# Performance work log

Measured on AMD Instinct MI355X. Metric: run time of the kernel, lower is better.

Reference implementation:

```python
import jax, jax.numpy as jnp
import numpy as np

E = 768
H = 12
D = E // H  # head_dim = 64
EPS = 1e-6
SCALE = D ** -0.5


def _l2norm(x, eps=EPS):
    # torch F.normalize: x / clamp_min(||x||_2, eps)
    n = jnp.sqrt(jnp.sum(x * x, axis=-1, keepdims=True))
    return x / jnp.maximum(n, eps)


def setup_inputs() -> dict:
    key = jax.random.key(0)
    ks = jax.random.split(key, 12)
    B, S = 2, 2048
    w = lambda k: jax.random.normal(k, (E, E), dtype=jnp.float32) * 0.02
    b = lambda k: jax.random.normal(k, (E,), dtype=jnp.float32) * 0.02
    return {
        "query": jax.random.normal(ks[0], (B, S, E), dtype=jnp.float32),
        "key": jax.random.normal(ks[1], (B, S, E), dtype=jnp.float32),
        "value": jax.random.normal(ks[2], (B, S, E), dtype=jnp.float32),
        "Wq": w(ks[3]), "bq": b(ks[4]),
        "Wk": w(ks[5]), "bk": b(ks[6]),
        "Wv": w(ks[7]), "bv": b(ks[8]),
        "Wo": w(ks[9]), "bo": b(ks[10]),
    }


def reference(query, key, value, Wq, bq, Wk, bk, Wv, bv, Wo, bo):
    B, T, _ = query.shape
    S = key.shape[1]
    # nn.Linear: x @ W.T + b; then split heads -> [B, H, S, D]
    split = lambda x, L: x.reshape(B, L, H, D).transpose(0, 2, 1, 3)
    q = split(query @ Wq.T + bq, T)
    k = split(key @ Wk.T + bk, S)
    v = split(value @ Wv.T + bv, S)
    q = _l2norm(q)
    k = _l2norm(k)
    scores = jnp.einsum("bhtd,bhsd->bhts", q, k) * SCALE
    attn = jax.nn.softmax(scores, axis=-1)
    ctx = jnp.einsum("bhts,bhsd->bhtd", attn, v)
    ctx = ctx.transpose(0, 2, 1, 3).reshape(B, T, E)
    return ctx @ Wo.T + bo
```

## Files before the change

### kernel.cpp

```cpp
#include <hip/hip_runtime.h>
#include <hip/hip_bf16.h>

#define EE 768
#define HH 12
#define DD 64
#define BB 2
#define SS 2048
#define MM (BB*SS)
#define NT (MM*EE)
#define NW (EE*EE)

typedef short short8 __attribute__((ext_vector_type(8)));
typedef float f32x4 __attribute__((ext_vector_type(4)));

static __device__ __forceinline__ unsigned short f2bf(float f) {
    unsigned int u = __float_as_uint(f);
    u += 0x7fffu + ((u >> 16) & 1u);
    return (unsigned short)(u >> 16);
}

static __device__ __forceinline__ void gl16(const void* g, void* l) {
    __builtin_amdgcn_global_load_lds(
        (const __attribute__((address_space(1))) unsigned int*)g,
        (__attribute__((address_space(3))) unsigned int*)l, 16, 0, 0);
}

static __device__ __forceinline__ int swz(int row, int chunk) {
    return row * 128 + ((chunk ^ (row & 7)) << 4);
}

__global__ __launch_bounds__(256) void cvt_x_kernel(
    const float* __restrict__ a0, const float* __restrict__ a1, const float* __restrict__ a2,
    unsigned short* __restrict__ o0, unsigned short* __restrict__ o1, unsigned short* __restrict__ o2)
{
    const float* s = (blockIdx.y == 0) ? a0 : (blockIdx.y == 1) ? a1 : a2;
    unsigned short* d = (blockIdx.y == 0) ? o0 : (blockIdx.y == 1) ? o1 : o2;
    const int idx = blockIdx.x * 256 + threadIdx.x;
    float4 f = ((const float4*)s)[idx];
    ushort4 u;
    u.x = f2bf(f.x); u.y = f2bf(f.y); u.z = f2bf(f.z); u.w = f2bf(f.w);
    ((ushort4*)d)[idx] = u;
}

__global__ __launch_bounds__(256) void cvt_w_kernel(
    const float* __restrict__ a0, const float* __restrict__ a1,
    const float* __restrict__ a2, const float* __restrict__ a3,
    unsigned short* __restrict__ o0, unsigned short* __restrict__ o1,
    unsigned short* __restrict__ o2, unsigned short* __restrict__ o3)
{
    const int y = blockIdx.y;
    const float* s = (y == 0) ? a0 : (y == 1) ? a1 : (y == 2) ? a2 : a3;
    unsigned short* d = (y == 0) ? o0 : (y == 1) ? o1 : (y == 2) ? o2 : o3;
    const int idx = blockIdx.x * 256 + threadIdx.x;
    float4 f = ((const float4*)s)[idx];
    ushort4 u;
    u.x = f2bf(f.x); u.y = f2bf(f.y); u.z = f2bf(f.z); u.w = f2bf(f.w);
    ((ushort4*)d)[idx] = u;
}

__global__ __launch_bounds__(256) void qkv_mfma_kernel(
    const unsigned short* __restrict__ xq, const unsigned short* __restrict__ xk,
    const unsigned short* __restrict__ xv,
    const unsigned short* __restrict__ Wq, const float* __restrict__ bq,
    const unsigned short* __restrict__ Wk, const float* __restrict__ bk,
    const unsigned short* __restrict__ Wv, const float* __restrict__ bv,
    unsigned short* __restrict__ qo, unsigned short* __restrict__ ko,
    unsigned short* __restrict__ vo)
{
    __shared__ short As[128 * 64];
    __shared__ short Bs[64 * 64];
    __shared__ float ssq[2][128];

    const int tid = threadIdx.x;
    const int bm  = blockIdx.x * 128;
    const int by  = blockIdx.y;
    const int proj = by / 12;
    const int h    = by % 12;
    const int n0r  = h * 64;

    const unsigned short* x = (proj == 0) ? xq : (proj == 1) ? xk : xv;
    const unsigned short* W = (proj == 0) ? Wq : (proj == 1) ? Wk : Wv;
    const float* bias       = (proj == 0) ? bq : (proj == 1) ? bk : bv;

    const int w  = tid >> 6;
    const int l  = tid & 63;
    const int c  = l & 15;
    const int g  = l >> 4;
    const int wm = w >> 1;
    const int wn = w & 1;
    const int lr8 = l >> 3;
    const int lc8 = (l & 7) ^ lr8;

    f32x4 acc[4][2] = {};

    for (int kt = 0; kt < EE; kt += 64) {
        __syncthreads();
        #pragma unroll
        for (int i = 0; i < 4; ++i) {
            const int t = w * 4 + i;
            const int row = t * 8 + lr8;
            gl16(x + (size_t)(bm + row) * EE + kt + lc8 * 8,
                 (unsigned short*)As + t * 512);
        }
        #pragma unroll
        for (int i = 0; i < 2; ++i) {
            const int t = w * 2 + i;
            const int row = t * 8 + lr8;
            gl16(W + (size_t)(n0r + row) * EE + kt + lc8 * 8,
                 (unsigned short*)Bs + t * 512);
        }
        __syncthreads();

        #pragma unroll
        for (int ks = 0; ks < 2; ++ks) {
            short8 bfr[2], afr[4];
            #pragma unroll
            for (int nt = 0; nt < 2; ++nt)
                bfr[nt] = *(const short8*)((const char*)Bs + swz(wn * 32 + nt * 16 + c, ks * 4 + g));
            #pragma unroll
            for (int mt = 0; mt < 4; ++mt)
                afr[mt] = *(const short8*)((const char*)As + swz(wm * 64 + mt * 16 + c, ks * 4 + g));
            #pragma unroll
            for (int mt = 0; mt < 4; ++mt)
                #pragma unroll
                for (int nt = 0; nt < 2; ++nt)
                    acc[mt][nt] = __builtin_amdgcn_mfma_f32_16x16x32_bf16(
                        afr[mt], bfr[nt], acc[mt][nt], 0, 0, 0);
        }
    }
    __syncthreads();

    float bb[2];
    #pragma unroll
    for (int nt = 0; nt < 2; ++nt) bb[nt] = bias[n0r + wn * 32 + nt * 16 + c];

    const int bidx  = bm >> 11;
    const int sbase = bm & (SS - 1);

    if (proj < 2) {
        f32x4 vr[4][2];
        f32x4 ssp[4];
        #pragma unroll
        for (int mt = 0; mt < 4; ++mt) {
            #pragma unroll
            for (int nt = 0; nt < 2; ++nt)
                #pragma unroll
                for (int j = 0; j < 4; ++j)
                    vr[mt][nt][j] = acc[mt][nt][j] + bb[nt];
            #pragma unroll
            for (int j = 0; j < 4; ++j)
                ssp[mt][j] = vr[mt][0][j]*vr[mt][0][j] + vr[mt][1][j]*vr[mt][1][j];
            #pragma unroll
            for (int j = 0; j < 4; ++j) {
                float s = ssp[mt][j];
                #pragma unroll
                for (int msk = 1; msk < 16; msk <<= 1) s += __shfl_xor(s, msk);
                ssp[mt][j] = s;
            }
        }
        if (c == 0) {
            #pragma unroll
            for (int mt = 0; mt < 4; ++mt)
                #pragma unroll
                for (int j = 0; j < 4; ++j)
                    ssq[wn][wm * 64 + mt * 16 + g * 4 + j] = ssp[mt][j];
        }
        __syncthreads();
        unsigned short* dst = (proj == 0) ? qo : ko;
        const float fold = (proj == 0) ? 0.125f : 1.0f;
        #pragma unroll
        for (int mt = 0; mt < 4; ++mt) {
            #pragma unroll
            for (int j = 0; j < 4; ++j) {
                const int rloc = wm * 64 + mt * 16 + g * 4 + j;
                const float ss = ssq[0][rloc] + ssq[1][rloc];
                const float inv = fold / fmaxf(sqrtf(ss), 1e-6f);
                const size_t base =
                    ((size_t)(bidx * HH + h) * SS + sbase + rloc) * DD;
                #pragma unroll
                for (int nt = 0; nt < 2; ++nt)
                    dst[base + wn * 32 + nt * 16 + c] = f2bf(vr[mt][nt][j] * inv);
            }
        }
    } else {
        #pragma unroll
        for (int mt = 0; mt < 4; ++mt)
            #pragma unroll
            for (int nt = 0; nt < 2; ++nt)
                #pragma unroll
                for (int j = 0; j < 4; ++j) {
                    const int row = wm * 64 + mt * 16 + g * 4 + j;
                    const int col = wn * 32 + nt * 16 + c;
                    As[row * 64 + col] = (short)f2bf(acc[mt][nt][j] + bb[nt]);
                }
        __syncthreads();
        const int d  = tid & 63;
        const int sb = (tid >> 6) * 32;
        unsigned short* dstp = vo + ((size_t)(bidx * HH + h) * DD + d) * SS + sbase + sb;
        #pragma unroll
        for (int grp = 0; grp < 4; ++grp) {
            unsigned int wds[4];
            #pragma unroll
            for (int e = 0; e < 4; ++e) {
                unsigned short u0 = (unsigned short)As[(sb + grp * 8 + 2 * e)     * 64 + d];
                unsigned short u1 = (unsigned short)As[(sb + grp * 8 + 2 * e + 1) * 64 + d];
                wds[e] = (unsigned int)u0 | ((unsigned int)u1 << 16);
            }
            int4 pk = make_int4((int)wds[0], (int)wds[1], (int)wds[2], (int)wds[3]);
            *(int4*)(dstp + grp * 8) = pk;
        }
    }
}

__global__ __launch_bounds__(128) void attn_mfma_kernel(
    const unsigned short* __restrict__ q, const unsigned short* __restrict__ k,
    const unsigned short* __restrict__ vT, unsigned short* __restrict__ ctx)
{
    __shared__ short Ks[64 * 64];
    __shared__ short Vs[64 * 64];
    __shared__ short Ps[2 * 32 * 64];

    const int tid = threadIdx.x;
    const int bh  = blockIdx.y;
    const int w   = tid >> 6;
    const int l   = tid & 63;
    const int c   = l & 15;
    const int g   = l >> 4;
    const int lr8 = l >> 3;
    const int lc8 = (l & 7) ^ lr8;
    const int qr0 = blockIdx.x * 64 + w * 32;

    short8 aq[2][2];
    #pragma unroll
    for (int m = 0; m < 2; ++m) {
        const unsigned short* qg = q + ((size_t)bh * SS + qr0 + m * 16 + c) * DD;
        aq[m][0] = *(const short8*)(qg + g * 8);
        aq[m][1] = *(const short8*)(qg + 32 + g * 8);
    }

    short* Psw = Ps + w * (32 * 64);
    f32x4 o[2][4] = {};
    f32x4 lsum[2] = {};

    for (int s0 = 0; s0 < SS; s0 += 64) {
        __syncthreads();
        #pragma unroll
        for (int i = 0; i < 4; ++i) {
            const int t = w * 4 + i;
            gl16(k + ((size_t)bh * SS + s0 + t * 8 + lr8) * DD + lc8 * 8,
                 (unsigned short*)Ks + t * 512);
        }
        #pragma unroll
        for (int i = 0; i < 4; ++i) {
            const int t = w * 4 + i;
            gl16(vT + ((size_t)bh * DD + t * 8 + lr8) * SS + s0 + lc8 * 8,
                 (unsigned short*)Vs + t * 512);
        }
        __syncthreads();

        f32x4 sc[2][4] = {};
        #pragma unroll
        for (int ks = 0; ks < 2; ++ks)
            #pragma unroll
            for (int nt = 0; nt < 4; ++nt) {
                short8 kf = *(const short8*)((const char*)Ks + swz(nt * 16 + c, ks * 4 + g));
                #pragma unroll
                for (int m = 0; m < 2; ++m)
                    sc[m][nt] = __builtin_amdgcn_mfma_f32_16x16x32_bf16(
                        aq[m][ks], kf, sc[m][nt], 0, 0, 0);
            }

        #pragma unroll
        for (int m = 0; m < 2; ++m) {
            f32x4 p[4];
            #pragma unroll
            for (int nt = 0; nt < 4; ++nt)
                #pragma unroll
                for (int j = 0; j < 4; ++j)
                    p[nt][j] = __expf(sc[m][nt][j]);
            #pragma unroll
            for (int j = 0; j < 4; ++j) {
                float r = p[0][j] + p[1][j] + p[2][j] + p[3][j];
                #pragma unroll
                for (int msk = 1; msk < 16; msk <<= 1) r += __shfl_xor(r, msk);
                lsum[m][j] += r;
            }
            #pragma unroll
            for (int nt = 0; nt < 4; ++nt)
                #pragma unroll
                for (int j = 0; j < 4; ++j) {
                    const int row = m * 16 + g * 4 + j;
                    const int ch  = (nt * 2 + (c >> 3)) ^ (row & 7);
                    Psw[row * 64 + (ch << 3) + (c & 7)] = (short)f2bf(p[nt][j]);
                }
        }

        #pragma unroll
        for (int ks = 0; ks < 2; ++ks) {
            short8 pa[2];
            #pragma unroll
            for (int m = 0; m < 2; ++m)
                pa[m] = *(const short8*)((const char*)Psw + swz(m * 16 + c, ks * 4 + g));
            #pragma unroll
            for (int dt = 0; dt < 4; ++dt) {
                short8 vf = *(const short8*)((const char*)Vs + swz(dt * 16 + c, ks * 4 + g));
                #pragma unroll
                for (int m = 0; m < 2; ++m)
                    o[m][dt] = __builtin_amdgcn_mfma_f32_16x16x32_bf16(
                        pa[m], vf, o[m][dt], 0, 0, 0);
            }
        }
    }

    const int bidx = bh / HH, h = bh % HH;
    #pragma unroll
    for (int m = 0; m < 2; ++m)
        #pragma unroll
        for (int j = 0; j < 4; ++j) {
            const float inv = 1.0f / lsum[m][j];
            const int sg = qr0 + m * 16 + g * 4 + j;
            unsigned short* op = ctx + ((size_t)bidx * SS + sg) * EE + h * DD + c;
            #pragma unroll
            for (int dt = 0; dt < 4; ++dt)
                op[dt * 16] = f2bf(o[m][dt][j] * inv);
        }
}

__global__ __launch_bounds__(256) void out_mfma_kernel(
    const unsigned short* __restrict__ A, const unsigned short* __restrict__ W,
    const float* __restrict__ bias, float* __restrict__ out)
{
    __shared__ short As[128 * 64];
    __shared__ short Bs[64 * 64];

    const int tid = threadIdx.x;
    const int bm  = blockIdx.x * 128;
    const int n0  = blockIdx.y * 64;

    const int w  = tid >> 6;
    const int l  = tid & 63;
    const int c  = l & 15;
    const int g  = l >> 4;
    const int wm = w >> 1;
    const int wn = w & 1;
    const int lr8 = l >> 3;
    const int lc8 = (l & 7) ^ lr8;

    f32x4 acc[4][2] = {};

    for (int kt = 0; kt < EE; kt += 64) {
        __syncthreads();
        #pragma unroll
        for (int i = 0; i < 4; ++i) {
            const int t = w * 4 + i;
            const int row = t * 8 + lr8;
            gl16(A + (size_t)(bm + row) * EE + kt + lc8 * 8,
                 (unsigned short*)As + t * 512);
        }
        #pragma unroll
        for (int i = 0; i < 2; ++i) {
            const int t = w * 2 + i;
            const int row = t * 8 + lr8;
            gl16(W + (size_t)(n0 + row) * EE + kt + lc8 * 8,
                 (unsigned short*)Bs + t * 512);
        }
        __syncthreads();

        #pragma unroll
        for (int ks = 0; ks < 2; ++ks) {
            short8 bfr[2], afr[4];
            #pragma unroll
            for (int nt = 0; nt < 2; ++nt)
                bfr[nt] = *(const short8*)((const char*)Bs + swz(wn * 32 + nt * 16 + c, ks * 4 + g));
            #pragma unroll
            for (int mt = 0; mt < 4; ++mt)
                afr[mt] = *(const short8*)((const char*)As + swz(wm * 64 + mt * 16 + c, ks * 4 + g));
            #pragma unroll
            for (int mt = 0; mt < 4; ++mt)
                #pragma unroll
                for (int nt = 0; nt < 2; ++nt)
                    acc[mt][nt] = __builtin_amdgcn_mfma_f32_16x16x32_bf16(
                        afr[mt], bfr[nt], acc[mt][nt], 0, 0, 0);
        }
    }

    float bb[2];
    #pragma unroll
    for (int nt = 0; nt < 2; ++nt) bb[nt] = bias[n0 + wn * 32 + nt * 16 + c];

    #pragma unroll
    for (int mt = 0; mt < 4; ++mt)
        #pragma unroll
        for (int j = 0; j < 4; ++j) {
            const int row = bm + wm * 64 + mt * 16 + g * 4 + j;
            float* op = out + (size_t)row * EE + n0 + wn * 32 + c;
            #pragma unroll
            for (int nt = 0; nt < 2; ++nt)
                op[nt * 16] = acc[mt][nt][j] + bb[nt];
        }
}

extern "C" void kernel_launch(void* const* d_in, const int* in_sizes, int n_in,
                              void* d_out, int out_size, void* d_ws, size_t ws_size,
                              hipStream_t stream)
{
    const float* query = (const float*)d_in[0];
    const float* key   = (const float*)d_in[1];
    const float* value = (const float*)d_in[2];
    const float* Wq = (const float*)d_in[3];
    const float* bq = (const float*)d_in[4];
    const float* Wk = (const float*)d_in[5];
    const float* bk = (const float*)d_in[6];
    const float* Wv = (const float*)d_in[7];
    const float* bv = (const float*)d_in[8];
    const float* Wo = (const float*)d_in[9];
    const float* bo = (const float*)d_in[10];
    float* out = (float*)d_out;

    unsigned short* xqc  = (unsigned short*)d_ws;
    unsigned short* xkc  = xqc  + NT;
    unsigned short* xvc  = xkc  + NT;
    unsigned short* qws  = xvc  + NT;
    unsigned short* kws  = qws  + NT;
    unsigned short* vtws = kws  + NT;
    unsigned short* wqc  = vtws + NT;
    unsigned short* wkc  = wqc  + NW;
    unsigned short* wvc  = wkc  + NW;
    unsigned short* woc  = wvc  + NW;
    unsigned short* ctx  = xqc;

    cvt_x_kernel<<<dim3(NT / 4 / 256, 3), 256, 0, stream>>>(
        query, key, value, xqc, xkc, xvc);
    cvt_w_kernel<<<dim3(NW / 4 / 256, 4), 256, 0, stream>>>(
        Wq, Wk, Wv, Wo, wqc, wkc, wvc, woc);
    qkv_mfma_kernel<<<dim3(MM / 128, 36), 256, 0, stream>>>(
        xqc, xkc, xvc, wqc, bq, wkc, bk, wvc, bv, qws, kws, vtws);
    attn_mfma_kernel<<<dim3(SS / 64, BB * HH), 128, 0, stream>>>(
        qws, kws, vtws, ctx);
    out_mfma_kernel<<<dim3(MM / 128, EE / 64), 256, 0, stream>>>(
        ctx, woc, bo, out);
}
```

Before: 235.2 us.

## Double-buffer LDS tiles in GEMM and attention kernels, merge conversion launches

```diff
diff --git a/kernel.cpp b/kernel.cpp
--- a/kernel.cpp
+++ b/kernel.cpp
@@ -29,33 +29,54 @@
     return row * 128 + ((chunk ^ (row & 7)) << 4);
 }
 
-__global__ __launch_bounds__(256) void cvt_x_kernel(
-    const float* __restrict__ a0, const float* __restrict__ a1, const float* __restrict__ a2,
-    unsigned short* __restrict__ o0, unsigned short* __restrict__ o1, unsigned short* __restrict__ o2)
-{
-    const float* s = (blockIdx.y == 0) ? a0 : (blockIdx.y == 1) ? a1 : a2;
-    unsigned short* d = (blockIdx.y == 0) ? o0 : (blockIdx.y == 1) ? o1 : o2;
+__global__ __launch_bounds__(256) void cvt_all_kernel(
+    const float* __restrict__ xq, const float* __restrict__ xk, const float* __restrict__ xv,
+    const float* __restrict__ wq, const float* __restrict__ wk,
+    const float* __restrict__ wv, const float* __restrict__ wo,
+    unsigned short* __restrict__ oq, unsigned short* __restrict__ ok, unsigned short* __restrict__ ov,
+    unsigned short* __restrict__ owq, unsigned short* __restrict__ owk,
+    unsigned short* __restrict__ owv, unsigned short* __restrict__ owo)
+{
+    const int XQ = NT / 4;
+    const int WQ = NW / 4;
     const int idx = blockIdx.x * 256 + threadIdx.x;
-    float4 f = ((const float4*)s)[idx];
+    const float* s;
+    unsigned short* d;
+    int off;
+    if (idx < 3 * XQ) {
+        const int r = idx / XQ;
+        off = idx - r * XQ;
+        s = (r == 0) ? xq : (r == 1) ? xk : xv;
+        d = (r == 0) ? oq : (r == 1) ? ok : ov;
+    } else {
+        const int j = idx - 3 * XQ;
+        const int r = j / WQ;
+        off = j - r * WQ;
+        s = (r == 0) ? wq : (r == 1) ? wk : (r == 2) ? wv : wo;
+        d = (r == 0) ? owq : (r == 1) ? owk : (r == 2) ? owv : owo;
+    }
+    float4 f = ((const float4*)s)[off];
     ushort4 u;
     u.x = f2bf(f.x); u.y = f2bf(f.y); u.z = f2bf(f.z); u.w = f2bf(f.w);
-    ((ushort4*)d)[idx] = u;
-}
-
-__global__ __launch_bounds__(256) void cvt_w_kernel(
-    const float* __restrict__ a0, const float* __restrict__ a1,
-    const float* __restrict__ a2, const float* __restrict__ a3,
-    unsigned short* __restrict__ o0, unsigned short* __restrict__ o1,
-    unsigned short* __restrict__ o2, unsigned short* __restrict__ o3)
-{
-    const int y = blockIdx.y;
-    const float* s = (y == 0) ? a0 : (y == 1) ? a1 : (y == 2) ? a2 : a3;
-    unsigned short* d = (y == 0) ? o0 : (y == 1) ? o1 : (y == 2) ? o2 : o3;
-    const int idx = blockIdx.x * 256 + threadIdx.x;
-    float4 f = ((const float4*)s)[idx];
-    ushort4 u;
-    u.x = f2bf(f.x); u.y = f2bf(f.y); u.z = f2bf(f.z); u.w = f2bf(f.w);
-    ((ushort4*)d)[idx] = u;
+    ((ushort4*)d)[off] = u;
+}
+
+static __device__ __forceinline__ void stage_ab(
+    const unsigned short* __restrict__ x, const unsigned short* __restrict__ W,
+    int bm, int n0, int kt, short* Abuf, short* Bbuf, int w, int lr8, int lc8)
+{
+    #pragma unroll
+    for (int i = 0; i < 4; ++i) {
+        const int t = w * 4 + i;
+        gl16(x + (size_t)(bm + t * 8 + lr8) * EE + kt + lc8 * 8,
+             (unsigned short*)Abuf + t * 512);
+    }
+    #pragma unroll
+    for (int i = 0; i < 2; ++i) {
+        const int t = w * 2 + i;
+        gl16(W + (size_t)(n0 + t * 8 + lr8) * EE + kt + lc8 * 8,
+             (unsigned short*)Bbuf + t * 512);
+    }
 }
 
 __global__ __launch_bounds__(256) void qkv_mfma_kernel(
@@ -67,8 +88,8 @@
     unsigned short* __restrict__ qo, unsigned short* __restrict__ ko,
     unsigned short* __restrict__ vo)
 {
-    __shared__ short As[128 * 64];
-    __shared__ short Bs[64 * 64];
+    __shared__ short As[2][128 * 64];
+    __shared__ short Bs[2][64 * 64];
     __shared__ float ssq[2][128];
 
     const int tid = threadIdx.x;
@@ -93,33 +114,23 @@
 
     f32x4 acc[4][2] = {};
 
-    for (int kt = 0; kt < EE; kt += 64) {
-        __syncthreads();
-        #pragma unroll
-        for (int i = 0; i < 4; ++i) {
-            const int t = w * 4 + i;
-            const int row = t * 8 + lr8;
-            gl16(x + (size_t)(bm + row) * EE + kt + lc8 * 8,
-                 (unsigned short*)As + t * 512);
-        }
-        #pragma unroll
-        for (int i = 0; i < 2; ++i) {
-            const int t = w * 2 + i;
-            const int row = t * 8 + lr8;
-            gl16(W + (size_t)(n0r + row) * EE + kt + lc8 * 8,
-                 (unsigned short*)Bs + t * 512);
-        }
-        __syncthreads();
+    stage_ab(x, W, bm, n0r, 0, As[0], Bs[0], w, lr8, lc8);
+    __syncthreads();
+
+    for (int it = 0; it < EE / 64; ++it) {
+        const int cur = it & 1;
+        if (it + 1 < EE / 64)
+            stage_ab(x, W, bm, n0r, (it + 1) * 64, As[cur ^ 1], Bs[cur ^ 1], w, lr8, lc8);
 
         #pragma unroll
         for (int ks = 0; ks < 2; ++ks) {
             short8 bfr[2], afr[4];
             #pragma unroll
             for (int nt = 0; nt < 2; ++nt)
-                bfr[nt] = *(const short8*)((const char*)Bs + swz(wn * 32 + nt * 16 + c, ks * 4 + g));
+                bfr[nt] = *(const short8*)((const char*)Bs[cur] + swz(wn * 32 + nt * 16 + c, ks * 4 + g));
             #pragma unroll
             for (int mt = 0; mt < 4; ++mt)
-                afr[mt] = *(const short8*)((const char*)As + swz(wm * 64 + mt * 16 + c, ks * 4 + g));
+                afr[mt] = *(const short8*)((const char*)As[cur] + swz(wm * 64 + mt * 16 + c, ks * 4 + g));
             #pragma unroll
             for (int mt = 0; mt < 4; ++mt)
                 #pragma unroll
@@ -127,8 +138,8 @@
                     acc[mt][nt] = __builtin_amdgcn_mfma_f32_16x16x32_bf16(
                         afr[mt], bfr[nt], acc[mt][nt], 0, 0, 0);
         }
-    }
-    __syncthreads();
+        __syncthreads();
+    }
 
     float bb[2];
     #pragma unroll
@@ -183,6 +194,7 @@
             }
         }
     } else {
+        short* T = As[0];
         #pragma unroll
         for (int mt = 0; mt < 4; ++mt)
             #pragma unroll
@@ -191,7 +203,7 @@
                 for (int j = 0; j < 4; ++j) {
                     const int row = wm * 64 + mt * 16 + g * 4 + j;
                     const int col = wn * 32 + nt * 16 + c;
-                    As[row * 64 + col] = (short)f2bf(acc[mt][nt][j] + bb[nt]);
+                    T[row * 64 + col] = (short)f2bf(acc[mt][nt][j] + bb[nt]);
                 }
         __syncthreads();
         const int d  = tid & 63;
@@ -202,13 +214,31 @@
             unsigned int wds[4];
             #pragma unroll
             for (int e = 0; e < 4; ++e) {
-                unsigned short u0 = (unsigned short)As[(sb + grp * 8 + 2 * e)     * 64 + d];
-                unsigned short u1 = (unsigned short)As[(sb + grp * 8 + 2 * e + 1) * 64 + d];
+                unsigned short u0 = (unsigned short)T[(sb + grp * 8 + 2 * e)     * 64 + d];
+                unsigned short u1 = (unsigned short)T[(sb + grp * 8 + 2 * e + 1) * 64 + d];
                 wds[e] = (unsigned int)u0 | ((unsigned int)u1 << 16);
             }
             int4 pk = make_int4((int)wds[0], (int)wds[1], (int)wds[2], (int)wds[3]);
             *(int4*)(dstp + grp * 8) = pk;
         }
+    }
+}
+
+static __device__ __forceinline__ void stage_kv(
+    const unsigned short* __restrict__ kbase, const unsigned short* __restrict__ vbase,
+    int s0, short* Kbuf, short* Vbuf, int w, int lr8, int lc8)
+{
+    #pragma unroll
+    for (int i = 0; i < 4; ++i) {
+        const int t = w * 4 + i;
+        gl16(kbase + (size_t)(s0 + t * 8 + lr8) * DD + lc8 * 8,
+             (unsigned short*)Kbuf + t * 512);
+    }
+    #pragma unroll
+    for (int i = 0; i < 4; ++i) {
+        const int t = w * 4 + i;
+        gl16(vbase + (size_t)(t * 8 + lr8) * SS + s0 + lc8 * 8,
+             (unsigned short*)Vbuf + t * 512);
     }
 }
 
@@ -216,8 +246,8 @@
     const unsigned short* __restrict__ q, const unsigned short* __restrict__ k,
     const unsigned short* __restrict__ vT, unsigned short* __restrict__ ctx)
 {
-    __shared__ short Ks[64 * 64];
-    __shared__ short Vs[64 * 64];
+    __shared__ short Ks[2][64 * 64];
+    __shared__ short Vs[2][64 * 64];
     __shared__ short Ps[2 * 32 * 64];
 
     const int tid = threadIdx.x;
@@ -230,6 +260,9 @@
     const int lc8 = (l & 7) ^ lr8;
     const int qr0 = blockIdx.x * 64 + w * 32;
 
+    const unsigned short* kbase = k  + (size_t)bh * SS * DD;
+    const unsigned short* vbase = vT + (size_t)bh * DD * SS;
+
     short8 aq[2][2];
     #pragma unroll
     for (int m = 0; m < 2; ++m) {
@@ -242,28 +275,20 @@
     f32x4 o[2][4] = {};
     f32x4 lsum[2] = {};
 
-    for (int s0 = 0; s0 < SS; s0 += 64) {
-        __syncthreads();
-        #pragma unroll
-        for (int i = 0; i < 4; ++i) {
-            const int t = w * 4 + i;
-            gl16(k + ((size_t)bh * SS + s0 + t * 8 + lr8) * DD + lc8 * 8,
-                 (unsigned short*)Ks + t * 512);
-        }
-        #pragma unroll
-        for (int i = 0; i < 4; ++i) {
-            const int t = w * 4 + i;
-            gl16(vT + ((size_t)bh * DD + t * 8 + lr8) * SS + s0 + lc8 * 8,
-                 (unsigned short*)Vs + t * 512);
-        }
-        __syncthreads();
+    stage_kv(kbase, vbase, 0, Ks[0], Vs[0], w, lr8, lc8);
+    __syncthreads();
+
+    for (int t = 0; t < SS / 64; ++t) {
+        const int cur = t & 1;
+        if (t + 1 < SS / 64)
+            stage_kv(kbase, vbase, (t + 1) * 64, Ks[cur ^ 1], Vs[cur ^ 1], w, lr8, lc8);
 
         f32x4 sc[2][4] = {};
         #pragma unroll
         for (int ks = 0; ks < 2; ++ks)
             #pragma unroll
             for (int nt = 0; nt < 4; ++nt) {
-                short8 kf = *(const short8*)((const char*)Ks + swz(nt * 16 + c, ks * 4 + g));
+                short8 kf = *(const short8*)((const char*)Ks[cur] + swz(nt * 16 + c, ks * 4 + g));
                 #pragma unroll
                 for (int m = 0; m < 2; ++m)
                     sc[m][nt] = __builtin_amdgcn_mfma_f32_16x16x32_bf16(
@@ -303,13 +328,14 @@
                 pa[m] = *(const short8*)((const char*)Psw + swz(m * 16 + c, ks * 4 + g));
             #pragma unroll
             for (int dt = 0; dt < 4; ++dt) {
-                short8 vf = *(const short8*)((const char*)Vs + swz(dt * 16 + c, ks * 4 + g));
+                short8 vf = *(const short8*)((const char*)Vs[cur] + swz(dt * 16 + c, ks * 4 + g));
                 #pragma unroll
                 for (int m = 0; m < 2; ++m)
                     o[m][dt] = __builtin_amdgcn_mfma_f32_16x16x32_bf16(
                         pa[m], vf, o[m][dt], 0, 0, 0);
             }
         }
+        __syncthreads();
     }
 
     const int bidx = bh / HH, h = bh % HH;
@@ -330,8 +356,8 @@
     const unsigned short* __restrict__ A, const unsigned short* __restrict__ W,
     const float* __restrict__ bias, float* __restrict__ out)
 {
-    __shared__ short As[128 * 64];
-    __shared__ short Bs[64 * 64];
+    __shared__ short As[2][128 * 64];
+    __shared__ short Bs[2][64 * 64];
 
     const int tid = threadIdx.x;
     const int bm  = blockIdx.x * 128;
@@ -348,33 +374,23 @@
 
     f32x4 acc[4][2] = {};
 
-    for (int kt = 0; kt < EE; kt += 64) {
-        __syncthreads();
-        #pragma unroll
-        for (int i = 0; i < 4; ++i) {
-            const int t = w * 4 + i;
-            const int row = t * 8 + lr8;
-            gl16(A + (size_t)(bm + row) * EE + kt + lc8 * 8,
-                 (unsigned short*)As + t * 512);
-        }
-        #pragma unroll
-        for (int i = 0; i < 2; ++i) {
-            const int t = w * 2 + i;
-            const int row = t * 8 + lr8;
-            gl16(W + (size_t)(n0 + row) * EE + kt + lc8 * 8,
-                 (unsigned short*)Bs + t * 512);
-        }
-        __syncthreads();
+    stage_ab(A, W, bm, n0, 0, As[0], Bs[0], w, lr8, lc8);
+    __syncthreads();
+
+    for (int it = 0; it < EE / 64; ++it) {
+        const int cur = it & 1;
+        if (it + 1 < EE / 64)
+            stage_ab(A, W, bm, n0, (it + 1) * 64, As[cur ^ 1], Bs[cur ^ 1], w, lr8, lc8);
 
         #pragma unroll
         for (int ks = 0; ks < 2; ++ks) {
             short8 bfr[2], afr[4];
             #pragma unroll
             for (int nt = 0; nt < 2; ++nt)
-                bfr[nt] = *(const short8*)((const char*)Bs + swz(wn * 32 + nt * 16 + c, ks * 4 + g));
+                bfr[nt] = *(const short8*)((const char*)Bs[cur] + swz(wn * 32 + nt * 16 + c, ks * 4 + g));
             #pragma unroll
             for (int mt = 0; mt < 4; ++mt)
-                afr[mt] = *(const short8*)((const char*)As + swz(wm * 64 + mt * 16 + c, ks * 4 + g));
+                afr[mt] = *(const short8*)((const char*)As[cur] + swz(wm * 64 + mt * 16 + c, ks * 4 + g));
             #pragma unroll
             for (int mt = 0; mt < 4; ++mt)
                 #pragma unroll
@@ -382,6 +398,7 @@
                     acc[mt][nt] = __builtin_amdgcn_mfma_f32_16x16x32_bf16(
                         afr[mt], bfr[nt], acc[mt][nt], 0, 0, 0);
         }
+        __syncthreads();
     }
 
     float bb[2];
@@ -429,10 +446,10 @@
     unsigned short* woc  = wvc  + NW;
     unsigned short* ctx  = xqc;
 
-    cvt_x_kernel<<<dim3(NT / 4 / 256, 3), 256, 0, stream>>>(
-        query, key, value, xqc, xkc, xvc);
-    cvt_w_kernel<<<dim3(NW / 4 / 256, 4), 256, 0, stream>>>(
-        Wq, Wk, Wv, Wo, wqc, wkc, wvc, woc);
+    const int cvt_blocks = (3 * (NT / 4) + 4 * (NW / 4)) / 256;
+    cvt_all_kernel<<<dim3(cvt_blocks), 256, 0, stream>>>(
+        query, key, value, Wq, Wk, Wv, Wo,
+        xqc, xkc, xvc, wqc, wkc, wvc, woc);
     qkv_mfma_kernel<<<dim3(MM / 128, 36), 256, 0, stream>>>(
         xqc, xkc, xvc, wqc, bq, wkc, bk, wvc, bv, qws, kws, vtws);
     attn_mfma_kernel<<<dim3(SS / 64, BB * HH), 128, 0, stream>>>(
```

Result: no change. 234.6 us (-0.2%).
